# Optimization experiments

Measured on AMD Instinct MI355X. Metric: run time of the kernel, lower is better.

## Reference

```python
import jax, jax.numpy as jnp
import numpy as np


def _init_linear(key, out_c, in_c):
    k1, k2 = jax.random.split(key)
    bound = 1.0 / np.sqrt(in_c)
    w = jax.random.uniform(k1, (out_c, in_c), jnp.float32, -bound, bound)
    b = jax.random.uniform(k2, (out_c,), jnp.float32, -bound, bound)
    return w, b


def setup_inputs() -> dict:
    key = jax.random.key(0)
    ks = jax.random.split(key, 8)
    N, E = 500000, 10000000
    x = jax.random.normal(ks[0], (N, 2), jnp.float32)
    edge_index = jax.random.randint(ks[1], (2, E), 0, N, jnp.int64)
    edge_attr = jax.random.normal(ks[2], (E, 1), jnp.float32)
    # EdgeCentric(2, 4, 1, 2)
    e1_fcx_w, e1_fcx_b = _init_linear(ks[3], 4, 2)
    e1_fce_w, e1_fce_b = _init_linear(ks[4], 2, 1)
    # NodeCentric(2, 4, 6, 10)
    n1_fcx_w, n1_fcx_b = _init_linear(ks[5], 4, 2)
    n1_fce_w, n1_fce_b = _init_linear(ks[6], 10, 6)
    return {
        "x": x, "edge_attr": edge_attr, "edge_index": edge_index,
        "e1_fcx_w": e1_fcx_w, "e1_fcx_b": e1_fcx_b,
        "e1_fce_w": e1_fce_w, "e1_fce_b": e1_fce_b,
        "n1_fcx_w": n1_fcx_w, "n1_fcx_b": n1_fcx_b,
        "n1_fce_w": n1_fce_w, "n1_fce_b": n1_fce_b,
    }


def reference(x, edge_attr, edge_index,
              e1_fcx_w, e1_fcx_b, e1_fce_w, e1_fce_b,
              n1_fcx_w, n1_fcx_b, n1_fce_w, n1_fce_b):
    N = x.shape[0]
    src, dst = edge_index[0], edge_index[1]
    # --- EdgeCentric: new edge features ---
    ea = edge_attr @ e1_fce_w.T + e1_fce_b              # [E, 2]
    node_sum = x[src] + x[dst]                          # [E, 2] gather over edges
    node_sum = node_sum @ e1_fcx_w.T + e1_fcx_b         # [E, 4]
    edge_attr2 = jax.nn.relu(jnp.concatenate([ea, node_sum], axis=1))  # [E, 6]
    # --- NodeCentric: new node features ---
    xn = x @ n1_fcx_w.T + n1_fcx_b                      # [N, 4]
    edge_sum = jax.ops.segment_sum(edge_attr2, src, num_segments=N)    # [N, 6] scatter-add
    edge_sum = edge_sum @ n1_fce_w.T + n1_fce_b         # [N, 10]
    x2 = jax.nn.relu(jnp.concatenate([xn, edge_sum], axis=1))          # [N, 14]
    return x2, edge_attr2
```

## Files before the change

### kernel.cpp

```cpp
#include <hip/hip_runtime.h>


#define NWGE      4096
#define CHUNK_MAX 2444
#define NPCB      2048
#define RS        8.0f
#define RS_INV    0.125f
#define XCD_SWZ(wg) ((((wg) & 7) * (NWGE / 8)) + ((wg) >> 3))

typedef float vfloat4 __attribute__((ext_vector_type(4)));
typedef float vfloat2 __attribute__((ext_vector_type(2)));
typedef int   vint4   __attribute__((ext_vector_type(4)));

__global__ __launch_bounds__(256) void sgnn_count(
    const int* __restrict__ src_idx,
    unsigned* __restrict__ cnt,
    int E, int NBC, int chunk)
{
    __shared__ unsigned hist[256];
    const int tid = threadIdx.x;
    const int cidx = XCD_SWZ(blockIdx.x);
    hist[tid] = 0u;
    __syncthreads();
    const int start = cidx * chunk;
    const int end   = min(E, start + chunk);
    for (int e = start + tid; e < end; e += 256)
        atomicAdd(&hist[((unsigned)src_idx[e]) >> 11], 1u);
    __syncthreads();
    if (tid < NBC) cnt[(size_t)tid * NWGE + cidx] = hist[tid];
}

__global__ __launch_bounds__(1024) void sgnn_scan_wg(
    const unsigned* __restrict__ cnt,
    unsigned* __restrict__ base,
    unsigned* __restrict__ btot)
{
    __shared__ unsigned p[1024];
    const int b = blockIdx.x, t = threadIdx.x;
    const size_t o = (size_t)b * NWGE + 4 * t;
    unsigned a[4];
    #pragma unroll
    for (int k = 0; k < 4; ++k) a[k] = cnt[o + k];
    const unsigned s = a[0] + a[1] + a[2] + a[3];
    p[t] = s;
    __syncthreads();
    for (int off = 1; off < 1024; off <<= 1) {
        const unsigned v = (t >= off) ? p[t - off] : 0u;
        __syncthreads();
        p[t] += v;
        __syncthreads();
    }
    unsigned run = p[t] - s;
    #pragma unroll
    for (int k = 0; k < 4; ++k) { base[o + k] = run; run += a[k]; }
    if (t == 1023) btot[b] = p[1023];
}

__global__ __launch_bounds__(256) void sgnn_scan_b(
    const unsigned* __restrict__ btot, unsigned* __restrict__ bbase, int NBC)
{
    __shared__ unsigned p[256];
    const int t = threadIdx.x;
    const unsigned v = (t < NBC) ? btot[t] : 0u;
    p[t] = v;
    __syncthreads();
    for (int off = 1; off < 256; off <<= 1) {
        const unsigned w = (t >= off) ? p[t - off] : 0u;
        __syncthreads();
        p[t] += w;
        __syncthreads();
    }
    if (t < NBC) bbase[t] = p[t] - v;
    if (t == 255) bbase[NBC] = p[255];
}

__global__ __launch_bounds__(256) void sgnn_emit_sort(
    const float* __restrict__ x,
    const float* __restrict__ edge_attr,
    const int*   __restrict__ src_idx,
    const int*   __restrict__ dst_idx,
    const float* __restrict__ e_fcx_w, const float* __restrict__ e_fcx_b,
    const float* __restrict__ e_fce_w, const float* __restrict__ e_fce_b,
    float* __restrict__ edge_out,
    const unsigned* __restrict__ base,
    const unsigned* __restrict__ bbase,
    unsigned long long* __restrict__ paybuf,
    int E, int NBC, int chunk)
{
    __shared__ unsigned long long srt[CHUNK_MAX];
    __shared__ unsigned short     perm[CHUNK_MAX];
    __shared__ unsigned hist[256];
    __shared__ unsigned runs[256];
    __shared__ int      dbase[256];

    const int tid = threadIdx.x;
    const int cidx = XCD_SWZ(blockIdx.x);
    hist[tid] = 0u;

    const int start = cidx * chunk;
    const int csize = min(E - start, chunk);
    const int iters = (chunk + 255) >> 8;

    const float we0 = e_fce_w[0], we1 = e_fce_w[1];
    const float be0 = e_fce_b[0], be1 = e_fce_b[1];
    const float wx00 = e_fcx_w[0], wx01 = e_fcx_w[1];
    const float wx10 = e_fcx_w[2], wx11 = e_fcx_w[3];
    const float wx20 = e_fcx_w[4], wx21 = e_fcx_w[5];
    const float wx30 = e_fcx_w[6], wx31 = e_fcx_w[7];
    const float bx0 = e_fcx_b[0], bx1 = e_fcx_b[1];
    const float bx2 = e_fcx_b[2], bx3 = e_fcx_b[3];

    __syncthreads();

    for (int it = 0; it < iters; ++it) {
        const int li = it * 256 + tid;
        if (li < csize) {
            const int e = start + li;
            const int s = src_idx[e];
            const int d = dst_idx[e];
            const float a = edge_attr[e];
            const float2 xs = *(const float2*)(x + 2 * (size_t)s);
            const float2 xd = *(const float2*)(x + 2 * (size_t)d);
            const float s0 = xs.x + xd.x, s1 = xs.y + xd.y;
            float o[6];
            o[0] = fmaxf(fmaf(a, we0, be0), 0.f);
            o[1] = fmaxf(fmaf(a, we1, be1), 0.f);
            o[2] = fmaxf(fmaf(s1, wx01, fmaf(s0, wx00, bx0)), 0.f);
            o[3] = fmaxf(fmaf(s1, wx11, fmaf(s0, wx10, bx1)), 0.f);
            o[4] = fmaxf(fmaf(s1, wx21, fmaf(s0, wx20, bx2)), 0.f);
            o[5] = fmaxf(fmaf(s1, wx31, fmaf(s0, wx30, bx3)), 0.f);

            vfloat2* eo = (vfloat2*)(edge_out + 6 * (size_t)e);
            vfloat2 w0 = { o[0], o[1] }, w1 = { o[2], o[3] }, w2 = { o[4], o[5] };
            __builtin_nontemporal_store(w0, eo + 0);
            __builtin_nontemporal_store(w1, eo + 1);
            __builtin_nontemporal_store(w2, eo + 2);

            unsigned long long rec = (unsigned long long)(unsigned)s << 42;
            #pragma unroll
            for (int f = 0; f < 6; ++f) {
                unsigned q = (unsigned)fmaf(o[f], RS, 0.5f);
                q = q > 127u ? 127u : q;
                rec |= (unsigned long long)q << (7 * f);
            }
            srt[li] = rec;
            atomicAdd(&hist[((unsigned)s) >> 11], 1u);
        }
    }
    __syncthreads();

    const unsigned v0 = hist[tid];
    for (int off = 1; off < 256; off <<= 1) {
        const unsigned w = (tid >= off) ? hist[tid - off] : 0u;
        __syncthreads();
        hist[tid] += w;
        __syncthreads();
    }
    const unsigned rstart = hist[tid] - v0;
    runs[tid] = rstart;
    if (tid < NBC)
        dbase[tid] = (int)(bbase[tid] + base[(size_t)tid * NWGE + cidx]) - (int)rstart;
    __syncthreads();

    for (int it = 0; it < iters; ++it) {
        const int li = it * 256 + tid;
        if (li < csize) {
            const unsigned b = (unsigned)(srt[li] >> 53);
            const unsigned pos = atomicAdd(&runs[b], 1u);
            perm[pos] = (unsigned short)li;
        }
    }
    __syncthreads();

    for (int it = 0; it < iters; ++it) {
        const int j = it * 256 + tid;
        if (j < csize) {
            const unsigned long long rec = srt[perm[j]];
            const unsigned b = (unsigned)(rec >> 53);
            paybuf[(unsigned)(dbase[b] + j)] = rec;
        }
    }
}

__global__ __launch_bounds__(1024) void sgnn_agg(
    const float* __restrict__ x,
    const unsigned* __restrict__ bbase,
    const unsigned long long* __restrict__ paybuf,
    const float* __restrict__ n_fcx_w, const float* __restrict__ n_fcx_b,
    const float* __restrict__ n_fce_w, const float* __restrict__ n_fce_b,
    float* __restrict__ x_out,
    int N)
{
    __shared__ __attribute__((aligned(16))) unsigned long long acc[NPCB][2];
    const int b = blockIdx.x, tid = threadIdx.x;
    for (int i = tid; i < NPCB; i += 1024) { acc[i][0] = 0ull; acc[i][1] = 0ull; }
    __syncthreads();

    const unsigned lo = bbase[b], hi = bbase[b + 1];
    for (unsigned i = lo + tid; i < hi; i += 1024) {
        const unsigned long long r = __builtin_nontemporal_load(paybuf + i);
        const unsigned id = (unsigned)(r >> 42) & 2047u;
        const unsigned long long l64 =
            ( r        & 127ull) | (((r >>  7) & 127ull) << 21) | (((r >> 14) & 127ull) << 42);
        const unsigned long long h64 =
            ((r >> 21) & 127ull) | (((r >> 28) & 127ull) << 21) | (((r >> 35) & 127ull) << 42);
        atomicAdd(&acc[id][0], l64);
        atomicAdd(&acc[id][1], h64);
    }
    __syncthreads();

    float wx[8], bx[4], we[60], be[10];
    #pragma unroll
    for (int k = 0; k < 8; ++k)  wx[k] = n_fcx_w[k];
    #pragma unroll
    for (int k = 0; k < 4; ++k)  bx[k] = n_fcx_b[k];
    #pragma unroll
    for (int k = 0; k < 60; ++k) we[k] = n_fce_w[k];
    #pragma unroll
    for (int k = 0; k < 10; ++k) be[k] = n_fce_b[k];

    for (int l = tid; l < NPCB; l += 1024) {
        const int n = b * NPCB + l;
        if (n >= N) break;
        const unsigned long long q0 = acc[l][0];
        const unsigned long long q1 = acc[l][1];
        float es[6];
        es[0] = (float)((unsigned)( q0       ) & 0x1FFFFFu) * RS_INV;
        es[1] = (float)((unsigned)( q0 >> 21 ) & 0x1FFFFFu) * RS_INV;
        es[2] = (float)((unsigned)( q0 >> 42 ) & 0x1FFFFFu) * RS_INV;
        es[3] = (float)((unsigned)( q1       ) & 0x1FFFFFu) * RS_INV;
        es[4] = (float)((unsigned)( q1 >> 21 ) & 0x1FFFFFu) * RS_INV;
        es[5] = (float)((unsigned)( q1 >> 42 ) & 0x1FFFFFu) * RS_INV;

        const float2 xv = *(const float2*)(x + 2 * (size_t)n);
        float out[14];
        #pragma unroll
        for (int k = 0; k < 4; ++k)
            out[k] = fmaxf(fmaf(xv.y, wx[2*k+1], fmaf(xv.x, wx[2*k], bx[k])), 0.f);
        #pragma unroll
        for (int j = 0; j < 10; ++j) {
            float t = be[j];
            #pragma unroll
            for (int i = 0; i < 6; ++i) t = fmaf(es[i], we[6*j+i], t);
            out[4 + j] = fmaxf(t, 0.f);
        }
        float2* o = (float2*)(x_out + 14 * (size_t)n);
        #pragma unroll
        for (int k = 0; k < 7; ++k) o[k] = make_float2(out[2*k], out[2*k+1]);
    }
}


#define SC6      16.0f
#define SC6_INV  0.0625f

__device__ __forceinline__ unsigned long long pack6(const float* o) {
    unsigned long long r = 0;
    #pragma unroll
    for (int k = 0; k < 6; ++k) {
        unsigned int q = (unsigned int)fmaf(o[k], SC6, 0.5f);
        r |= (unsigned long long)q << (10 * k);
    }
    return r;
}

__global__ __launch_bounds__(256) void sgnn_edge_xcd(
    const float* __restrict__ x, const float* __restrict__ edge_attr,
    const int* __restrict__ src_idx, const int* __restrict__ dst_idx,
    const float* __restrict__ e_fcx_w, const float* __restrict__ e_fcx_b,
    const float* __restrict__ e_fce_w, const float* __restrict__ e_fce_b,
    float* __restrict__ edge_out, unsigned long long* __restrict__ accq8,
    int E, int N)
{
    unsigned int xcd;
    asm("s_getreg_b32 %0, hwreg(HW_REG_XCC_ID, 0, 32)" : "=s"(xcd));
    unsigned long long* __restrict__ acc = accq8 + (size_t)(xcd & 7) * N;

    const float we0 = e_fce_w[0], we1 = e_fce_w[1];
    const float be0 = e_fce_b[0], be1 = e_fce_b[1];
    const float wx00 = e_fcx_w[0], wx01 = e_fcx_w[1];
    const float wx10 = e_fcx_w[2], wx11 = e_fcx_w[3];
    const float wx20 = e_fcx_w[4], wx21 = e_fcx_w[5];
    const float wx30 = e_fcx_w[6], wx31 = e_fcx_w[7];
    const float bx0 = e_fcx_b[0], bx1 = e_fcx_b[1];
    const float bx2 = e_fcx_b[2], bx3 = e_fcx_b[3];

    const int E2 = E >> 1;
    const int stride = gridDim.x * blockDim.x;
    for (int p = blockIdx.x * blockDim.x + threadIdx.x; p < E2; p += stride) {
        const int e = 2 * p;
        const int2   ss = *(const int2*)(src_idx + e);
        const int2   dd = *(const int2*)(dst_idx + e);
        const float2 aa = *(const float2*)(edge_attr + e);
        float v[12];
        #pragma unroll
        for (int i = 0; i < 2; ++i) {
            const int s = i ? ss.y : ss.x;
            const int d = i ? dd.y : dd.x;
            const float a = i ? aa.y : aa.x;
            const float2 xs = *(const float2*)(x + 2 * s);
            const float2 xd = *(const float2*)(x + 2 * d);
            const float s0 = xs.x + xd.x, s1 = xs.y + xd.y;
            float* o = v + 6 * i;
            o[0] = fmaxf(fmaf(a, we0, be0), 0.f);
            o[1] = fmaxf(fmaf(a, we1, be1), 0.f);
            o[2] = fmaxf(fmaf(s1, wx01, fmaf(s0, wx00, bx0)), 0.f);
            o[3] = fmaxf(fmaf(s1, wx11, fmaf(s0, wx10, bx1)), 0.f);
            o[4] = fmaxf(fmaf(s1, wx21, fmaf(s0, wx20, bx2)), 0.f);
            o[5] = fmaxf(fmaf(s1, wx31, fmaf(s0, wx30, bx3)), 0.f);
            __hip_atomic_fetch_add(acc + s, pack6(o),
                                   __ATOMIC_RELAXED, __HIP_MEMORY_SCOPE_WORKGROUP);
        }
        vfloat4* dst4 = (vfloat4*)(edge_out + 6 * e);
        vfloat4 w0 = { v[0], v[1], v[2],  v[3] };
        vfloat4 w1 = { v[4], v[5], v[6],  v[7] };
        vfloat4 w2 = { v[8], v[9], v[10], v[11] };
        __builtin_nontemporal_store(w0, dst4 + 0);
        __builtin_nontemporal_store(w1, dst4 + 1);
        __builtin_nontemporal_store(w2, dst4 + 2);
    }
    if ((E & 1) && blockIdx.x == 0 && threadIdx.x == 0) {
        const int e = E - 1;
        const int s = src_idx[e], d = dst_idx[e];
        const float a = edge_attr[e];
        const float2 xs = *(const float2*)(x + 2 * s);
        const float2 xd = *(const float2*)(x + 2 * d);
        const float s0 = xs.x + xd.x, s1 = xs.y + xd.y;
        float o[6];
        o[0] = fmaxf(fmaf(a, we0, be0), 0.f);
        o[1] = fmaxf(fmaf(a, we1, be1), 0.f);
        o[2] = fmaxf(fmaf(s1, wx01, fmaf(s0, wx00, bx0)), 0.f);
        o[3] = fmaxf(fmaf(s1, wx11, fmaf(s0, wx10, bx1)), 0.f);
        o[4] = fmaxf(fmaf(s1, wx21, fmaf(s0, wx20, bx2)), 0.f);
        o[5] = fmaxf(fmaf(s1, wx31, fmaf(s0, wx30, bx3)), 0.f);
        #pragma unroll
        for (int k = 0; k < 6; ++k) edge_out[6 * e + k] = o[k];
        __hip_atomic_fetch_add(acc + s, pack6(o),
                               __ATOMIC_RELAXED, __HIP_MEMORY_SCOPE_WORKGROUP);
    }
}

__global__ __launch_bounds__(256) void sgnn_node_xcd(
    const float* __restrict__ x, const unsigned long long* __restrict__ accq8,
    const float* __restrict__ n_fcx_w, const float* __restrict__ n_fcx_b,
    const float* __restrict__ n_fce_w, const float* __restrict__ n_fce_b,
    float* __restrict__ x_out, int N)
{
    float wx[8], bx[4], we[60], be[10];
    #pragma unroll
    for (int k = 0; k < 8; ++k)  wx[k] = n_fcx_w[k];
    #pragma unroll
    for (int k = 0; k < 4; ++k)  bx[k] = n_fcx_b[k];
    #pragma unroll
    for (int k = 0; k < 60; ++k) we[k] = n_fce_w[k];
    #pragma unroll
    for (int k = 0; k < 10; ++k) be[k] = n_fce_b[k];

    const int stride = gridDim.x * blockDim.x;
    for (int n = blockIdx.x * blockDim.x + threadIdx.x; n < N; n += stride) {
        unsigned int f[6] = {0, 0, 0, 0, 0, 0};
        #pragma unroll
        for (int xb = 0; xb < 8; ++xb) {
            const unsigned long long q = accq8[(size_t)xb * N + n];
            f[0] += (unsigned int)(q)       & 0x3FFu;
            f[1] += (unsigned int)(q >> 10) & 0x3FFu;
            f[2] += (unsigned int)(q >> 20) & 0x3FFu;
            f[3] += (unsigned int)(q >> 30) & 0x3FFu;
            f[4] += (unsigned int)(q >> 40) & 0x3FFu;
            f[5] += (unsigned int)(q >> 50);
        }
        float es[6];
        #pragma unroll
        for (int k = 0; k < 6; ++k) es[k] = (float)f[k] * SC6_INV;
        const float2 xv = *(const float2*)(x + 2 * n);
        float out[14];
        #pragma unroll
        for (int k = 0; k < 4; ++k)
            out[k] = fmaxf(fmaf(xv.y, wx[2*k+1], fmaf(xv.x, wx[2*k], bx[k])), 0.f);
        #pragma unroll
        for (int j = 0; j < 10; ++j) {
            float t = be[j];
            #pragma unroll
            for (int i = 0; i < 6; ++i) t = fmaf(es[i], we[6*j+i], t);
            out[4 + j] = fmaxf(t, 0.f);
        }
        float2* o = (float2*)(x_out + 14 * n);
        #pragma unroll
        for (int k = 0; k < 7; ++k) o[k] = make_float2(out[2*k], out[2*k+1]);
    }
}

extern "C" void kernel_launch(void* const* d_in, const int* in_sizes, int n_in,
                              void* d_out, int out_size, void* d_ws, size_t ws_size,
                              hipStream_t stream) {
    const float* x          = (const float*)d_in[0];
    const float* edge_attr  = (const float*)d_in[1];
    const int*   edge_index = (const int*)d_in[2];
    const float* e_fcx_w    = (const float*)d_in[3];
    const float* e_fcx_b    = (const float*)d_in[4];
    const float* e_fce_w    = (const float*)d_in[5];
    const float* e_fce_b    = (const float*)d_in[6];
    const float* n_fcx_w    = (const float*)d_in[7];
    const float* n_fcx_b    = (const float*)d_in[8];
    const float* n_fce_w    = (const float*)d_in[9];
    const float* n_fce_b    = (const float*)d_in[10];

    const int N = in_sizes[0] / 2;
    const int E = in_sizes[1];

    float* x_out    = (float*)d_out;
    float* edge_out = (float*)d_out + (size_t)N * 14;

    const int* src_idx = edge_index;
    const int* dst_idx = edge_index + E;

    const int NBC = (N + NPCB - 1) / NPCB;
    const int chunk = (E + NWGE - 1) / NWGE;

    const size_t szCnt   = (size_t)NBC * NWGE * 4;
    const size_t offBtot = (szCnt + 255) & ~(size_t)255;
    const size_t offBB   = offBtot + 4096;
    const size_t offPay  = offBB + 4096;
    const size_t need    = offPay + (size_t)E * 8;

    if (NBC <= 255 && chunk <= CHUNK_MAX && ws_size >= need) {
        unsigned* cnt   = (unsigned*)d_ws;
        unsigned* btot  = (unsigned*)((char*)d_ws + offBtot);
        unsigned* bbase = (unsigned*)((char*)d_ws + offBB);
        unsigned long long* paybuf = (unsigned long long*)((char*)d_ws + offPay);

        sgnn_count<<<NWGE, 256, 0, stream>>>(src_idx, cnt, E, NBC, chunk);
        sgnn_scan_wg<<<NBC, 1024, 0, stream>>>(cnt, cnt, btot);
        sgnn_scan_b<<<1, 256, 0, stream>>>(btot, bbase, NBC);
        sgnn_emit_sort<<<NWGE, 256, 0, stream>>>(
            x, edge_attr, src_idx, dst_idx,
            e_fcx_w, e_fcx_b, e_fce_w, e_fce_b,
            edge_out, cnt, bbase, paybuf, E, NBC, chunk);
        sgnn_agg<<<NBC, 1024, 0, stream>>>(
            x, bbase, paybuf,
            n_fcx_w, n_fcx_b, n_fce_w, n_fce_b, x_out, N);
    } else {
        unsigned long long* accq8 = (unsigned long long*)d_ws;
        (void)hipMemsetAsync(accq8, 0, (size_t)8 * N * sizeof(unsigned long long), stream);
        sgnn_edge_xcd<<<8192, 256, 0, stream>>>(
            x, edge_attr, src_idx, dst_idx,
            e_fcx_w, e_fcx_b, e_fce_w, e_fce_b,
            edge_out, accq8, E, N);
        sgnn_node_xcd<<<1024, 256, 0, stream>>>(
            x, accq8, n_fcx_w, n_fcx_b, n_fce_w, n_fce_b, x_out, N);
    }
}
```

Measured before the change: 230.1 us.

## Gather bf16-packed node features and vectorize edge loads/stores four-wide

Adds a pre-pass that packs each node's two float features into one 32-bit word of two rounded bf16 values, so the src/dst gathers in the edge kernel fetch 4 bytes instead of 8. The count and emit kernels now process four edges per thread with 128-bit nontemporal loads of indices and attributes, and write edge outputs and sort records as wide vectors. Chunk size is rounded to a multiple of four to keep the vector accesses aligned. Using bf16 inputs changes the edge_attr2 outputs numerically and may exceed tolerance, and the extra kernel launch and workspace use add some overhead.

```diff
diff --git a/kernel.cpp b/kernel.cpp
--- a/kernel.cpp
+++ b/kernel.cpp
@@ -11,6 +11,24 @@
 typedef float vfloat4 __attribute__((ext_vector_type(4)));
 typedef float vfloat2 __attribute__((ext_vector_type(2)));
 typedef int   vint4   __attribute__((ext_vector_type(4)));
+typedef unsigned long long vull2 __attribute__((ext_vector_type(2)));
+
+__global__ __launch_bounds__(256) void sgnn_xq(
+    const float* __restrict__ x, unsigned* __restrict__ xq, int N)
+{
+    const int stride = gridDim.x * blockDim.x;
+    for (int i = blockIdx.x * blockDim.x + threadIdx.x; i < N; i += stride) {
+        const float2 v = *(const float2*)(x + 2 * (size_t)i);
+        const unsigned b0 = (__float_as_uint(v.x) + 0x8000u) >> 16;
+        const unsigned b1 = (__float_as_uint(v.y) + 0x8000u) & 0xffff0000u;
+        xq[i] = b0 | b1;
+    }
+}
+
+__device__ __forceinline__ void xq_unpack(unsigned p, float& a, float& b) {
+    a = __uint_as_float(p << 16);
+    b = __uint_as_float(p & 0xffff0000u);
+}
 
 __global__ __launch_bounds__(256) void sgnn_count(
     const int* __restrict__ src_idx,
@@ -24,8 +42,17 @@
     __syncthreads();
     const int start = cidx * chunk;
     const int end   = min(E, start + chunk);
-    for (int e = start + tid; e < end; e += 256)
-        atomicAdd(&hist[((unsigned)src_idx[e]) >> 11], 1u);
+    for (int e0 = start + tid * 4; e0 < end; e0 += 1024) {
+        if (e0 + 4 <= end) {
+            const vint4 s4 = __builtin_nontemporal_load((const vint4*)(src_idx + e0));
+            #pragma unroll
+            for (int k = 0; k < 4; ++k)
+                atomicAdd(&hist[((unsigned)s4[k]) >> 11], 1u);
+        } else {
+            for (int e = e0; e < end; ++e)
+                atomicAdd(&hist[((unsigned)src_idx[e]) >> 11], 1u);
+        }
+    }
     __syncthreads();
     if (tid < NBC) cnt[(size_t)tid * NWGE + cidx] = hist[tid];
 }
@@ -75,7 +102,7 @@
 }
 
 __global__ __launch_bounds__(256) void sgnn_emit_sort(
-    const float* __restrict__ x,
+    const unsigned* __restrict__ xq,
     const float* __restrict__ edge_attr,
     const int*   __restrict__ src_idx,
     const int*   __restrict__ dst_idx,
@@ -87,7 +114,7 @@
     unsigned long long* __restrict__ paybuf,
     int E, int NBC, int chunk)
 {
-    __shared__ unsigned long long srt[CHUNK_MAX];
+    __shared__ __attribute__((aligned(16))) unsigned long long srt[CHUNK_MAX];
     __shared__ unsigned short     perm[CHUNK_MAX];
     __shared__ unsigned hist[256];
     __shared__ unsigned runs[256];
@@ -112,39 +139,83 @@
 
     __syncthreads();
 
-    for (int it = 0; it < iters; ++it) {
-        const int li = it * 256 + tid;
-        if (li < csize) {
-            const int e = start + li;
-            const int s = src_idx[e];
-            const int d = dst_idx[e];
-            const float a = edge_attr[e];
-            const float2 xs = *(const float2*)(x + 2 * (size_t)s);
-            const float2 xd = *(const float2*)(x + 2 * (size_t)d);
-            const float s0 = xs.x + xd.x, s1 = xs.y + xd.y;
-            float o[6];
-            o[0] = fmaxf(fmaf(a, we0, be0), 0.f);
-            o[1] = fmaxf(fmaf(a, we1, be1), 0.f);
-            o[2] = fmaxf(fmaf(s1, wx01, fmaf(s0, wx00, bx0)), 0.f);
-            o[3] = fmaxf(fmaf(s1, wx11, fmaf(s0, wx10, bx1)), 0.f);
-            o[4] = fmaxf(fmaf(s1, wx21, fmaf(s0, wx20, bx2)), 0.f);
-            o[5] = fmaxf(fmaf(s1, wx31, fmaf(s0, wx30, bx3)), 0.f);
-
-            vfloat2* eo = (vfloat2*)(edge_out + 6 * (size_t)e);
-            vfloat2 w0 = { o[0], o[1] }, w1 = { o[2], o[3] }, w2 = { o[4], o[5] };
-            __builtin_nontemporal_store(w0, eo + 0);
-            __builtin_nontemporal_store(w1, eo + 1);
-            __builtin_nontemporal_store(w2, eo + 2);
-
-            unsigned long long rec = (unsigned long long)(unsigned)s << 42;
+    const int iters4 = (chunk + 1023) >> 10;
+    for (int it = 0; it < iters4; ++it) {
+        const int li0 = (it << 10) + tid * 4;
+        if (li0 + 4 <= csize) {
+            const int e0 = start + li0;
+            const vint4   s4 = __builtin_nontemporal_load((const vint4*)(src_idx + e0));
+            const vint4   d4 = __builtin_nontemporal_load((const vint4*)(dst_idx + e0));
+            const vfloat4 a4 = __builtin_nontemporal_load((const vfloat4*)(edge_attr + e0));
+            unsigned ps[4], pd[4];
             #pragma unroll
-            for (int f = 0; f < 6; ++f) {
-                unsigned q = (unsigned)fmaf(o[f], RS, 0.5f);
-                q = q > 127u ? 127u : q;
-                rec |= (unsigned long long)q << (7 * f);
+            for (int k = 0; k < 4; ++k) { ps[k] = xq[(unsigned)s4[k]]; pd[k] = xq[(unsigned)d4[k]]; }
+
+            float v[24];
+            unsigned long long recs[4];
+            #pragma unroll
+            for (int k = 0; k < 4; ++k) {
+                float xs0, xs1, xd0, xd1;
+                xq_unpack(ps[k], xs0, xs1);
+                xq_unpack(pd[k], xd0, xd1);
+                const float s0 = xs0 + xd0, s1 = xs1 + xd1;
+                const float a = a4[k];
+                float* o = v + 6 * k;
+                o[0] = fmaxf(fmaf(a, we0, be0), 0.f);
+                o[1] = fmaxf(fmaf(a, we1, be1), 0.f);
+                o[2] = fmaxf(fmaf(s1, wx01, fmaf(s0, wx00, bx0)), 0.f);
+                o[3] = fmaxf(fmaf(s1, wx11, fmaf(s0, wx10, bx1)), 0.f);
+                o[4] = fmaxf(fmaf(s1, wx21, fmaf(s0, wx20, bx2)), 0.f);
+                o[5] = fmaxf(fmaf(s1, wx31, fmaf(s0, wx30, bx3)), 0.f);
+                unsigned long long rec = (unsigned long long)(unsigned)s4[k] << 42;
+                #pragma unroll
+                for (int f = 0; f < 6; ++f) {
+                    unsigned q = (unsigned)fmaf(o[f], RS, 0.5f);
+                    q = q > 127u ? 127u : q;
+                    rec |= (unsigned long long)q << (7 * f);
+                }
+                recs[k] = rec;
+                atomicAdd(&hist[((unsigned)s4[k]) >> 11], 1u);
             }
-            srt[li] = rec;
-            atomicAdd(&hist[((unsigned)s) >> 11], 1u);
+            vfloat4* eo = (vfloat4*)(edge_out + 6 * (size_t)e0);
+            #pragma unroll
+            for (int j = 0; j < 6; ++j) {
+                vfloat4 w = { v[4*j], v[4*j+1], v[4*j+2], v[4*j+3] };
+                __builtin_nontemporal_store(w, eo + j);
+            }
+            vull2* sp = (vull2*)&srt[li0];
+            vull2 r01 = { recs[0], recs[1] }, r23 = { recs[2], recs[3] };
+            sp[0] = r01; sp[1] = r23;
+        } else {
+            for (int k = 0; k < 4; ++k) {
+                const int li = li0 + k;
+                if (li >= csize) break;
+                const int e = start + li;
+                const int s = src_idx[e];
+                const float a = edge_attr[e];
+                float xs0, xs1, xd0, xd1;
+                xq_unpack(xq[(unsigned)s], xs0, xs1);
+                xq_unpack(xq[(unsigned)dst_idx[e]], xd0, xd1);
+                const float s0 = xs0 + xd0, s1 = xs1 + xd1;
+                float o[6];
+                o[0] = fmaxf(fmaf(a, we0, be0), 0.f);
+                o[1] = fmaxf(fmaf(a, we1, be1), 0.f);
+                o[2] = fmaxf(fmaf(s1, wx01, fmaf(s0, wx00, bx0)), 0.f);
+                o[3] = fmaxf(fmaf(s1, wx11, fmaf(s0, wx10, bx1)), 0.f);
+                o[4] = fmaxf(fmaf(s1, wx21, fmaf(s0, wx20, bx2)), 0.f);
+                o[5] = fmaxf(fmaf(s1, wx31, fmaf(s0, wx30, bx3)), 0.f);
+                #pragma unroll
+                for (int f = 0; f < 6; ++f) edge_out[6 * (size_t)e + f] = o[f];
+                unsigned long long rec = (unsigned long long)(unsigned)s << 42;
+                #pragma unroll
+                for (int f = 0; f < 6; ++f) {
+                    unsigned q = (unsigned)fmaf(o[f], RS, 0.5f);
+                    q = q > 127u ? 127u : q;
+                    rec |= (unsigned long long)q << (7 * f);
+                }
+                srt[li] = rec;
+                atomicAdd(&hist[((unsigned)s) >> 11], 1u);
+            }
         }
     }
     __syncthreads();
@@ -415,25 +486,29 @@
     const int* dst_idx = edge_index + E;
 
     const int NBC = (N + NPCB - 1) / NPCB;
-    const int chunk = (E + NWGE - 1) / NWGE;
-
+    int chunk = (E + NWGE - 1) / NWGE;
+    chunk = (chunk + 3) & ~3;
+
+    const size_t offCnt  = ((size_t)N * 4 + 255) & ~(size_t)255;
     const size_t szCnt   = (size_t)NBC * NWGE * 4;
-    const size_t offBtot = (szCnt + 255) & ~(size_t)255;
+    const size_t offBtot = offCnt + ((szCnt + 255) & ~(size_t)255);
     const size_t offBB   = offBtot + 4096;
     const size_t offPay  = offBB + 4096;
     const size_t need    = offPay + (size_t)E * 8;
 
     if (NBC <= 255 && chunk <= CHUNK_MAX && ws_size >= need) {
-        unsigned* cnt   = (unsigned*)d_ws;
+        unsigned* xq    = (unsigned*)d_ws;
+        unsigned* cnt   = (unsigned*)((char*)d_ws + offCnt);
         unsigned* btot  = (unsigned*)((char*)d_ws + offBtot);
         unsigned* bbase = (unsigned*)((char*)d_ws + offBB);
         unsigned long long* paybuf = (unsigned long long*)((char*)d_ws + offPay);
 
+        sgnn_xq<<<512, 256, 0, stream>>>(x, xq, N);
         sgnn_count<<<NWGE, 256, 0, stream>>>(src_idx, cnt, E, NBC, chunk);
         sgnn_scan_wg<<<NBC, 1024, 0, stream>>>(cnt, cnt, btot);
         sgnn_scan_b<<<1, 256, 0, stream>>>(btot, bbase, NBC);
         sgnn_emit_sort<<<NWGE, 256, 0, stream>>>(
-            x, edge_attr, src_idx, dst_idx,
+            xq, edge_attr, src_idx, dst_idx,
             e_fcx_w, e_fcx_b, e_fce_w, e_fce_b,
             edge_out, cnt, bbase, paybuf, E, NBC, chunk);
         sgnn_agg<<<NBC, 1024, 0, stream>>>(
```

New measurement: 414.6 us. 80.2% more time.
